# Kernel tuning notes

Hardware: AMD Instinct MI355X
Metric: run time of the kernel (lower is better)

Reference implementation:

```python
import jax, jax.numpy as jnp
import numpy as np

NUCLEIC_ACID_CUTOFF = 30.0
OTHER_CUTOFF = 15.0


def _cdist(x):
    # x: [b, n, 3] -> pairwise euclidean distances [b, n, n]
    sq = jnp.sum(x * x, axis=-1)  # [b, n]
    d2 = sq[:, :, None] + sq[:, None, :] - 2.0 * jnp.einsum('bid,bjd->bij', x, x)
    d2 = jnp.maximum(d2, 0.0)
    # safe sqrt (zero diagonal would produce nan grads otherwise)
    safe = jnp.where(d2 > 0.0, d2, 1.0)
    return jnp.where(d2 > 0.0, jnp.sqrt(safe), 0.0)


def setup_inputs() -> dict:
    key = jax.random.key(0)
    k1, k2, k3, k4, k5 = jax.random.split(key, 5)
    b, n = 2, 4096
    # scale ~10 Angstrom spread so distances straddle the 15/30 cutoffs
    true_coords = jax.random.normal(k1, (b, n, 3), dtype=jnp.float32) * 10.0
    pred_coords = true_coords + jax.random.normal(k2, (b, n, 3), dtype=jnp.float32) * 1.5
    is_dna = jax.random.bernoulli(k3, 0.15, (b, n))
    is_rna = jax.random.bernoulli(k4, 0.15, (b, n))
    coords_mask = jax.random.bernoulli(k5, 0.95, (b, n))
    return {
        'pred_coords': pred_coords,
        'true_coords': true_coords,
        'is_dna': is_dna,
        'is_rna': is_rna,
        'coords_mask': coords_mask,
    }


def reference(pred_coords, true_coords, is_dna, is_rna, coords_mask):
    n = pred_coords.shape[1]
    pred_dists = _cdist(pred_coords)  # [b, n, n]
    true_dists = _cdist(true_coords)  # [b, n, n]
    dist_diff = jnp.abs(true_dists - pred_dists)
    eps = (
        jax.nn.sigmoid(0.5 - dist_diff)
        + jax.nn.sigmoid(1.0 - dist_diff)
        + jax.nn.sigmoid(2.0 - dist_diff)
        + jax.nn.sigmoid(4.0 - dist_diff)
    ) / 4.0

    is_nucleotide = is_dna | is_rna  # [b, n]
    is_nucleotide_pair = is_nucleotide[:, :, None] & is_nucleotide[:, None, :]
    inclusion_radius = jnp.where(
        is_nucleotide_pair,
        true_dists < NUCLEIC_ACID_CUTOFF,
        true_dists < OTHER_CUTOFF,
    )
    not_eye = ~jnp.eye(n, dtype=bool)[None, :, :]
    mask = inclusion_radius & not_eye
    mask = mask & (coords_mask[:, :, None] & coords_mask[:, None, :])

    maskf = mask.astype(eps.dtype)
    lddt_sum = jnp.sum(eps * maskf, axis=(-1, -2))  # [b]
    lddt_count = jnp.sum(maskf, axis=(-1, -2))  # [b]
    lddt = lddt_sum / jnp.maximum(lddt_count, 1.0)
    return 1.0 - jnp.mean(lddt)
```

## Files before the change

kernel.cpp:

```cpp
#include <hip/hip_runtime.h>
#include <hip/hip_bf16.h>


#define NRES 4096
#define NBATCH 2
#define TJ 128
#define NBLOCKS (16 * 32 * NBATCH)

#define CUT15 21.6404256133f
#define CUT30 43.2808512267f

#define S1 66.35420923f
#define S2 678.60880385f
#define S3 2039.58217570f
#define S4 1808.04241445f
#define QP1 16.58855231f
#define QP2 339.30440193f
#define QP3 1529.68663177f
#define QP4 1808.04241445f

#define LOG2E 1.44269504089f

__global__ void pack_kernel(const float* __restrict__ pred,
                            const float* __restrict__ truec,
                            const int* __restrict__ dna,
                            const int* __restrict__ rna,
                            const int* __restrict__ cm,
                            float4* __restrict__ tp,
                            float4* __restrict__ pp)
{
    int idx = blockIdx.x * 256 + threadIdx.x;
    if (idx >= NRES * NBATCH) return;
    float nuc = ((dna[idx] | rna[idx]) != 0) ? 1.0f : 0.0f;
    float cmf = (cm[idx] != 0) ? 1.0f : 0.0f;
    tp[idx] = make_float4(truec[3*idx+0]*LOG2E, truec[3*idx+1]*LOG2E, truec[3*idx+2]*LOG2E, nuc);
    pp[idx] = make_float4(pred[3*idx+0]*LOG2E,  pred[3*idx+1]*LOG2E,  pred[3*idx+2]*LOG2E,  cmf);
}

#define K_LOOP(DIAG)                                                        \
    _Pragma("unroll 4")                                                     \
    for (int k = 0; k < TJ; ++k) {                                          \
        const float4 tj = stj[k];                                           \
        const float4 pj = spj[k];                                           \
        float dx = tix - tj.x, dy = tiy - tj.y, dz = tiz - tj.z;            \
        float dt = __builtin_amdgcn_sqrtf(dx*dx + dy*dy + dz*dz);           \
        float ex = pix - pj.x, ey = piy - pj.y, ez = piz - pj.z;            \
        float dp = __builtin_amdgcn_sqrtf(ex*ex + ey*ey + ez*ez);           \
        float cutoff = __builtin_fmaf(tj.w, cHiLo, cLo);                    \
        float mf = (dt < cutoff) ? pj.w : 0.0f;                             \
        if (DIAG) mf = (j0 + k > i) ? mf : 0.0f;                            \
        float t = __builtin_amdgcn_exp2f(-fabsf(dt - dp));                  \
        float Q  = 1.0f + t*(S1 + t*(S2 + t*(S3 + t*S4)));                  \
        float Qp = QP1 + t*(QP2 + t*(QP3 + t*QP4));                         \
        float rq = __builtin_amdgcn_rcpf(Q);                                \
        s += mf * ((t * Qp) * rq);                                          \
        c += mf;                                                            \
    }

__launch_bounds__(256, 4)
__global__ void lddt_main(const float4* __restrict__ tp,
                          const float4* __restrict__ pp,
                          float* __restrict__ acc,
                          unsigned int* __restrict__ done,
                          float* __restrict__ out)
{
    const int b   = blockIdx.z;
    const int bi  = blockIdx.x;
    const int cj  = blockIdx.y;
    const int tid = threadIdx.x;

    if (cj < 2 * bi) {
        if (tid == 0) {
            __threadfence();
            unsigned int old = atomicAdd(done, 1u);
            if (old == NBLOCKS - 1u) {
                float a0 = __hip_atomic_load(&acc[0], __ATOMIC_ACQUIRE, __HIP_MEMORY_SCOPE_AGENT);
                float a1 = __hip_atomic_load(&acc[1], __ATOMIC_ACQUIRE, __HIP_MEMORY_SCOPE_AGENT);
                float c0 = __hip_atomic_load(&acc[2], __ATOMIC_ACQUIRE, __HIP_MEMORY_SCOPE_AGENT);
                float c1 = __hip_atomic_load(&acc[3], __ATOMIC_ACQUIRE, __HIP_MEMORY_SCOPE_AGENT);
                float l0 = a0 / fmaxf(c0, 0.5f);
                float l1 = a1 / fmaxf(c1, 0.5f);
                out[0] = 1.0f - 0.5f * (l0 + l1);
            }
        }
        return;
    }

    const int base = b * NRES;
    const int j0   = cj * TJ;
    const int i    = bi * 256 + tid;

    __shared__ float4 stj[TJ];
    __shared__ float4 spj[TJ];
    if (tid < TJ) stj[tid]      = tp[base + j0 + tid];
    else          spj[tid - TJ] = pp[base + j0 + (tid - TJ)];

    const float4 ti4 = tp[base + i];
    const float4 pi4 = pp[base + i];
    const float tix = ti4.x, tiy = ti4.y, tiz = ti4.z;
    const float pix = pi4.x, piy = pi4.y, piz = pi4.z;
    const bool  cmi  = (pi4.w != 0.0f);
    const bool  nuci = (ti4.w != 0.0f);
    const float cHi = cmi ? (nuci ? CUT30 : CUT15) : -1.0f;
    const float cLo = cmi ? CUT15 : -1.0f;
    const float cHiLo = cHi - cLo;

    __syncthreads();

    float s = 0.0f, c = 0.0f;

    if (cj <= 2 * bi + 1) { K_LOOP(1) }
    else                  { K_LOOP(0) }

    #pragma unroll
    for (int off = 32; off > 0; off >>= 1) {
        s += __shfl_down(s, off, 64);
        c += __shfl_down(c, off, 64);
    }

    __shared__ float red_s[4];
    __shared__ float red_c[4];
    const int wid  = tid >> 6;
    const int lane = tid & 63;
    if (lane == 0) { red_s[wid] = s; red_c[wid] = c; }
    __syncthreads();

    if (tid == 0) {
        float ts = red_s[0] + red_s[1] + red_s[2] + red_s[3];
        float tc = red_c[0] + red_c[1] + red_c[2] + red_c[3];
        atomicAdd(&acc[b], ts);
        atomicAdd(&acc[NBATCH + b], tc);
        __threadfence();
        unsigned int old = atomicAdd(done, 1u);
        if (old == NBLOCKS - 1u) {
            float a0 = __hip_atomic_load(&acc[0], __ATOMIC_ACQUIRE, __HIP_MEMORY_SCOPE_AGENT);
            float a1 = __hip_atomic_load(&acc[1], __ATOMIC_ACQUIRE, __HIP_MEMORY_SCOPE_AGENT);
            float c0 = __hip_atomic_load(&acc[2], __ATOMIC_ACQUIRE, __HIP_MEMORY_SCOPE_AGENT);
            float c1 = __hip_atomic_load(&acc[3], __ATOMIC_ACQUIRE, __HIP_MEMORY_SCOPE_AGENT);
            float l0 = a0 / fmaxf(c0, 0.5f);
            float l1 = a1 / fmaxf(c1, 0.5f);
            out[0] = 1.0f - 0.5f * (l0 + l1);
        }
    }
}

extern "C" void kernel_launch(void* const* d_in, const int* in_sizes, int n_in,
                              void* d_out, int out_size, void* d_ws, size_t ws_size,
                              hipStream_t stream) {
    const float* pred  = (const float*)d_in[0];
    const float* truec = (const float*)d_in[1];
    const int*   dna   = (const int*)d_in[2];
    const int*   rna   = (const int*)d_in[3];
    const int*   cmask = (const int*)d_in[4];
    float* out = (float*)d_out;

    char* ws = (char*)d_ws;
    float*        acc  = (float*)ws;
    unsigned int* done = (unsigned int*)(ws + 64);
    float4* tp = (float4*)(ws + 1024);
    float4* pp = (float4*)(ws + 1024 + NBATCH*NRES*16);

    (void)hipMemsetAsync(ws, 0, 128, stream);

    pack_kernel<<<(NRES*NBATCH + 255)/256, 256, 0, stream>>>(pred, truec, dna, rna, cmask, tp, pp);

    dim3 grid(NRES / 256, NRES / TJ, NBATCH);
    lddt_main<<<grid, 256, 0, stream>>>(tp, pp, acc, done, out);
}
```

Baseline: 50.34 us.

## Launch only upper-triangle tiles with halved column tile and linear block mapping

Replaces the 3D grid, in which lower-triangle blocks exited early, with a compact 1D grid of only the active upper-triangle tiles. Each block finds its row and column tile from its linear index with a small loop. The column tile shrinks from 128 to 64 columns, so per-block work is finer and there are 1088 blocks instead of 1024. Launch bounds are raised to 6 waves per SIMD. This is meant to cut wasted block launches and improve load balance, at the cost of more per-block overhead, more atomics and extra register pressure.

```diff
diff --git a/kernel.cpp b/kernel.cpp
--- a/kernel.cpp
+++ b/kernel.cpp
@@ -4,8 +4,9 @@
 
 #define NRES 4096
 #define NBATCH 2
-#define TJ 128
-#define NBLOCKS (16 * 32 * NBATCH)
+#define TJ 64
+#define NACT 544
+#define NBLOCKS (NACT * NBATCH)
 
 #define CUT15 21.6404256133f
 #define CUT30 43.2808512267f
@@ -57,34 +58,20 @@
         c += mf;                                                            \
     }
 
-__launch_bounds__(256, 4)
+__launch_bounds__(256, 6)
 __global__ void lddt_main(const float4* __restrict__ tp,
                           const float4* __restrict__ pp,
                           float* __restrict__ acc,
                           unsigned int* __restrict__ done,
                           float* __restrict__ out)
 {
-    const int b   = blockIdx.z;
-    const int bi  = blockIdx.x;
-    const int cj  = blockIdx.y;
+    const int b   = blockIdx.y;
+    const int m   = blockIdx.x;
     const int tid = threadIdx.x;
 
-    if (cj < 2 * bi) {
-        if (tid == 0) {
-            __threadfence();
-            unsigned int old = atomicAdd(done, 1u);
-            if (old == NBLOCKS - 1u) {
-                float a0 = __hip_atomic_load(&acc[0], __ATOMIC_ACQUIRE, __HIP_MEMORY_SCOPE_AGENT);
-                float a1 = __hip_atomic_load(&acc[1], __ATOMIC_ACQUIRE, __HIP_MEMORY_SCOPE_AGENT);
-                float c0 = __hip_atomic_load(&acc[2], __ATOMIC_ACQUIRE, __HIP_MEMORY_SCOPE_AGENT);
-                float c1 = __hip_atomic_load(&acc[3], __ATOMIC_ACQUIRE, __HIP_MEMORY_SCOPE_AGENT);
-                float l0 = a0 / fmaxf(c0, 0.5f);
-                float l1 = a1 / fmaxf(c1, 0.5f);
-                out[0] = 1.0f - 0.5f * (l0 + l1);
-            }
-        }
-        return;
-    }
+    int bi = 0, C = 0;
+    while (C + (TJ - 4 * bi) <= m) { C += TJ - 4 * bi; ++bi; }
+    const int cj = 4 * bi + (m - C);
 
     const int base = b * NRES;
     const int j0   = cj * TJ;
@@ -92,8 +79,8 @@
 
     __shared__ float4 stj[TJ];
     __shared__ float4 spj[TJ];
-    if (tid < TJ) stj[tid]      = tp[base + j0 + tid];
-    else          spj[tid - TJ] = pp[base + j0 + (tid - TJ)];
+    if (tid < TJ)                stj[tid]      = tp[base + j0 + tid];
+    else if (tid < 2 * TJ)       spj[tid - TJ] = pp[base + j0 + (tid - TJ)];
 
     const float4 ti4 = tp[base + i];
     const float4 pi4 = pp[base + i];
@@ -109,8 +96,8 @@
 
     float s = 0.0f, c = 0.0f;
 
-    if (cj <= 2 * bi + 1) { K_LOOP(1) }
-    else                  { K_LOOP(0) }
+    if (cj < 4 * bi + 4) { K_LOOP(1) }
+    else                 { K_LOOP(0) }
 
     #pragma unroll
     for (int off = 32; off > 0; off >>= 1) {
@@ -164,6 +151,6 @@
 
     pack_kernel<<<(NRES*NBATCH + 255)/256, 256, 0, stream>>>(pred, truec, dna, rna, cmask, tp, pp);
 
-    dim3 grid(NRES / 256, NRES / TJ, NBATCH);
+    dim3 grid(NACT, NBATCH);
     lddt_main<<<grid, 256, 0, stream>>>(tp, pp, acc, done, out);
 }
```

Measured after the change: 52.03 us. +3.4%, slower.
